# Optimization experiments

Measured on AMD Instinct MI355X. Metric: run time of the kernel, lower is better.

Reference implementation:

```python
import jax, jax.numpy as jnp
import numpy as np
import math

B, S, D, H = 1, 2048, 4096, 32
HD = D // H  # 128
BASE = 10000.0
NEG = -1e9


def rotate_half(x):
    x1, x2 = x[..., : x.shape[-1] // 2], x[..., x.shape[-1] // 2 :]
    return jnp.concatenate((-x2, x1), axis=-1)


def setup_inputs() -> dict:
    key = jax.random.key(0)
    ks = jax.random.split(key, 5)
    scale = 1.0 / math.sqrt(D)
    hidden_states = jax.random.normal(ks[0], (B, S, D), dtype=jnp.float32)
    Wq = jax.random.normal(ks[1], (D, D), dtype=jnp.float32) * scale
    Wk = jax.random.normal(ks[2], (D, D), dtype=jnp.float32) * scale
    Wv = jax.random.normal(ks[3], (D, D), dtype=jnp.float32) * scale
    Wo = jax.random.normal(ks[4], (D, D), dtype=jnp.float32) * scale
    # causal additive mask [1,1,S,S]
    causal = jnp.tril(jnp.ones((S, S), dtype=bool))
    attention_mask = jnp.where(causal, 0.0, NEG).astype(jnp.float32)[None, None]
    # rotary cos/sin cache [1,1,S,HD]
    inv_freq = 1.0 / (BASE ** (jnp.arange(0, HD, 2, dtype=jnp.float32) / HD))
    freqs = jnp.arange(S, dtype=jnp.float32)[:, None] * inv_freq[None, :]
    emb = jnp.concatenate((freqs, freqs), axis=-1)
    cos = jnp.cos(emb)[None, None]
    sin = jnp.sin(emb)[None, None]
    return dict(hidden_states=hidden_states, attention_mask=attention_mask,
                cos=cos, sin=sin, Wq=Wq, Wk=Wk, Wv=Wv, Wo=Wo)


def reference(hidden_states, attention_mask, cos, sin, Wq, Wk, Wv, Wo):
    b, s, d = hidden_states.shape
    # projections (torch Linear: x @ W.T), reshape to [B,H,S,HD]
    def proj(W):
        return (hidden_states @ W.T).reshape(b, s, H, HD).transpose(0, 2, 1, 3)
    q, k, v = proj(Wq), proj(Wk), proj(Wv)
    # RoPE
    q = q * cos + rotate_half(q) * sin
    k = k * cos + rotate_half(k) * sin
    # scores [B,H,S,S], key pre-scaled as in original
    scores = jnp.einsum('bhqd,bhkd->bhqk', q, k / math.sqrt(HD)) + attention_mask
    attn = jax.nn.softmax(scores.astype(jnp.float32), axis=-1).astype(scores.dtype)
    out = jnp.einsum('bhqk,bhkd->bhqd', attn, v)
    out = out.transpose(0, 2, 1, 3).reshape(b, s, d)
    return out @ Wo.T
```

## Files before the change

kernel.cpp:

```cpp
#include <hip/hip_runtime.h>
#include <hip/hip_bf16.h>
#include <stdint.h>

#define DEV __device__ __forceinline__

typedef __bf16 bf16x8 __attribute__((ext_vector_type(8)));
typedef float f32x4 __attribute__((ext_vector_type(4)));
typedef unsigned short ushort8_t __attribute__((ext_vector_type(8)));
typedef unsigned short ushort4_t __attribute__((ext_vector_type(4)));

constexpr int S = 2048;
constexpr int D = 4096;
constexpr int H = 32;
constexpr int HD = 128;
constexpr float kSc = 0.08838834764831845f * 1.4426950408889634f;

DEV unsigned short f2bf(float f) {
    uint32_t u = __builtin_bit_cast(uint32_t, f);
    u += 0x7fffu + ((u >> 16) & 1u);
    return (unsigned short)(u >> 16);
}
DEV float bf2f(unsigned short h) {
    uint32_t u = ((uint32_t)h) << 16;
    return __builtin_bit_cast(float, u);
}

DEV void gload_lds16(const void* g, void* l) {
    __builtin_amdgcn_global_load_lds(
        (const __attribute__((address_space(1))) void*)g,
        (__attribute__((address_space(3))) void*)l,
        16, 0, 0);
}

DEV f32x4 mfma16(bf16x8 a, bf16x8 b, f32x4 c) {
    return __builtin_amdgcn_mfma_f32_16x16x32_bf16(a, b, c, 0, 0, 0);
}

__global__ __launch_bounds__(256) void cvt_all(const float* __restrict__ hs,
                                               const float* __restrict__ w0,
                                               const float* __restrict__ w1,
                                               const float* __restrict__ w2,
                                               const float* __restrict__ w3,
                                               unsigned short* __restrict__ hsb,
                                               unsigned short* __restrict__ o0,
                                               unsigned short* __restrict__ o1,
                                               unsigned short* __restrict__ o2,
                                               unsigned short* __restrict__ o3) {
    const int b = blockIdx.x;
    const float* in;
    unsigned short* out;
    size_t blk;
    if (b < 4096) {
        in = hs; out = hsb; blk = (size_t)b;
    } else {
        const int i = b - 4096;
        const int w = i >> 13;
        const int r = i & 8191;
        in  = (w == 0) ? w0 : (w == 1) ? w1 : (w == 2) ? w2 : w3;
        out = (w == 0) ? o0 : (w == 1) ? o1 : (w == 2) ? o2 : o3;
        blk = (size_t)r;
    }
    const size_t i8 = blk * 256 + threadIdx.x;
    f32x4 a = ((const f32x4*)in)[2 * i8];
    f32x4 c = ((const f32x4*)in)[2 * i8 + 1];
    ushort8_t o;
    o[0] = f2bf(a[0]); o[1] = f2bf(a[1]); o[2] = f2bf(a[2]); o[3] = f2bf(a[3]);
    o[4] = f2bf(c[0]); o[5] = f2bf(c[1]); o[6] = f2bf(c[2]); o[7] = f2bf(c[3]);
    ((ushort8_t*)out)[i8] = o;
}

template <int BN, int OMODE>
__global__ __launch_bounds__(512, 2) void gemm8(const unsigned short* __restrict__ Ap,
                                                const unsigned short* __restrict__ Bp,
                                                unsigned short* __restrict__ Oq,
                                                unsigned short* __restrict__ Ok,
                                                unsigned short* __restrict__ Ovt,
                                                float* __restrict__ Of) {
    constexpr int NT = BN / 64;
    constexpr int NB = BN / 64;
    extern __shared__ unsigned short lds8[];
    unsigned short (*As)[8192] = (unsigned short(*)[8192])lds8;
    unsigned short* Bs0 = lds8 + 4 * 8192;
    unsigned short* Bs1 = Bs0 + BN * 64;

    const int tix = threadIdx.x;
    const int lane = tix & 63;
    const int w = tix >> 6;
    const int g = lane >> 4;
    const int rl = lane & 15;
    const int wm = w >> 2;
    const int wn = w & 3;
    const int bc0 = wn * (BN / 4);
    const int rx = rl & 7;

    const int yy = blockIdx.x & 7;
    const int xx = blockIdx.x >> 3;
    const int m0 = yy * 256;
    const int n0 = xx * BN;

    int srowA[2], scolA[2];
#pragma unroll
    for (int u = 0; u < 2; ++u) {
        const int c = u * 512 + tix;
        srowA[u] = c >> 3;
        scolA[u] = ((c & 7) ^ (srowA[u] & 7)) << 3;
    }
    int srowB[NB], scolB[NB];
#pragma unroll
    for (int u = 0; u < NB; ++u) {
        const int c = u * 512 + tix;
        srowB[u] = c >> 3;
        scolB[u] = ((c & 7) ^ (srowB[u] & 7)) << 3;
    }

    const char* aBase[2] = {(const char*)As[wm], (const char*)As[2 + wm]};
    const char* bBase[2] = {(const char*)Bs0, (const char*)Bs1};

    f32x4 acc[4][2][NT] = {};
    bf16x8 bfr[NT][2];

#define STG_A8(t, h, slot)                                                        \
    if ((t) < 64) {                                                               \
        _Pragma("unroll") for (int u = 0; u < 2; ++u)                             \
            gload_lds16(Ap + (size_t)(m0 + (h) * 128 + srowA[u]) * 4096 +         \
                            (t) * 64 + scolA[u],                                  \
                        &As[slot][(u * 512 + tix) * 8]);                          \
    }
#define STG_B8(t, slot)                                                           \
    if ((t) < 64) {                                                               \
        unsigned short* bs_ = (slot) ? Bs1 : Bs0;                                 \
        _Pragma("unroll") for (int u = 0; u < NB; ++u)                            \
            gload_lds16(Bp + (size_t)(n0 + srowB[u]) * 4096 +                     \
                            (t) * 64 + scolB[u],                                  \
                        &bs_[(u * 512 + tix) * 8]);                               \
    }

#define PHASE8(pt, q, STG, VM)                                                    \
    {                                                                             \
        bf16x8 af[2][2];                                                          \
        _Pragma("unroll") for (int mi = 0; mi < 2; ++mi)                          \
        _Pragma("unroll") for (int ks = 0; ks < 2; ++ks) {                        \
            const int ab = ((q) * 32 + mi * 16 + rl) * 128 +                      \
                           ((((ks << 2) + g) ^ rx) << 4);                         \
            af[mi][ks] = *(const bf16x8*)(aBase[pt] + ab);                        \
        }                                                                         \
        if ((q) == 0) {                                                           \
            _Pragma("unroll") for (int nt = 0; nt < NT; ++nt)                     \
            _Pragma("unroll") for (int ks = 0; ks < 2; ++ks) {                    \
                const int bb = (bc0 + nt * 16 + rl) * 128 +                       \
                               ((((ks << 2) + g) ^ rx) << 4);                     \
                bfr[nt][ks] = *(const bf16x8*)(bBase[pt] + bb);                   \
            }                                                                     \
        }                                                                         \
        STG;                                                                      \
        if (VM) {                                                                 \
            if (last) {                                                           \
                asm volatile("s_waitcnt vmcnt(0)" ::: "memory");                  \
            } else if constexpr (NB == 3) {                                       \
                asm volatile("s_waitcnt vmcnt(3)" ::: "memory");                  \
            } else {                                                              \
                asm volatile("s_waitcnt vmcnt(2)" ::: "memory");                  \
            }                                                                     \
        }                                                                         \
        __builtin_amdgcn_s_barrier();                                             \
        __builtin_amdgcn_s_setprio(1);                                            \
        _Pragma("unroll") for (int ks = 0; ks < 2; ++ks)                          \
        _Pragma("unroll") for (int mi = 0; mi < 2; ++mi)                          \
        _Pragma("unroll") for (int nt = 0; nt < NT; ++nt)                         \
            acc[q][mi][nt] = mfma16(af[mi][ks], bfr[nt][ks], acc[q][mi][nt]);     \
        __builtin_amdgcn_s_setprio(0);                                            \
        __builtin_amdgcn_s_barrier();                                             \
    }

    STG_A8(0, 0, 0); STG_A8(0, 1, 1);
    STG_B8(0, 0); STG_B8(1, 1);
    __syncthreads();

    for (int i = 0; i < 32; ++i) {
        const bool last = (i == 31);
        const int o = 2 * i + 1, ne = 2 * i + 2, no = 2 * i + 3;
        PHASE8(0, 0, STG_A8(o, 0, 2), 0)
        PHASE8(0, 1, STG_A8(o, 1, 3), 0)
        PHASE8(0, 2, STG_B8(ne, 0), 0)
        PHASE8(0, 3, ((void)0), 1)
        PHASE8(1, 0, STG_A8(ne, 0, 0), 0)
        PHASE8(1, 1, STG_A8(ne, 1, 1), 0)
        PHASE8(1, 2, STG_B8(no, 1), 0)
        PHASE8(1, 3, ((void)0), 1)
    }
#undef PHASE8
#undef STG_A8
#undef STG_B8

#pragma unroll
    for (int q = 0; q < 4; ++q)
#pragma unroll
        for (int mi = 0; mi < 2; ++mi)
#pragma unroll
            for (int nt = 0; nt < NT; ++nt) {
                const int row0 = m0 + wm * 128 + q * 32 + mi * 16 + g * 4;
                const int gc = n0 + bc0 + nt * 16 + rl;
                if constexpr (OMODE == 0) {
                    const int sel = gc >> 12;
                    const int col = gc & 4095;
                    if (sel == 2) {
                        ushort4_t v;
#pragma unroll
                        for (int r = 0; r < 4; ++r) v[r] = f2bf(acc[q][mi][nt][r]);
                        *(ushort4_t*)&Ovt[(size_t)col * S + row0] = v;
                    } else {
                        unsigned short* op = sel ? Ok : Oq;
#pragma unroll
                        for (int r = 0; r < 4; ++r)
                            op[(size_t)(row0 + r) * 4096 + col] = f2bf(acc[q][mi][nt][r]);
                    }
                } else {
#pragma unroll
                    for (int r = 0; r < 4; ++r)
                        Of[(size_t)(row0 + r) * 4096 + gc] = acc[q][mi][nt][r];
                }
            }
}

__global__ __launch_bounds__(256) void rope_kernel(unsigned short* __restrict__ Qb,
                                                   unsigned short* __restrict__ Kb,
                                                   const float* __restrict__ cosT,
                                                   const float* __restrict__ sinT) {
    const int i = blockIdx.x * 256 + threadIdx.x;
    const int j8 = i & 7;
    const int h = (i >> 3) & 31;
    const int s = i >> 8;
    const size_t base = (size_t)s * D + h * HD + j8 * 8;
    const float* cp = cosT + s * HD + j8 * 8;
    const float* sp = sinT + s * HD + j8 * 8;
    float c1[8], s1[8], c2[8], s2[8];
#pragma unroll
    for (int k = 0; k < 8; ++k) { c1[k] = cp[k]; s1[k] = sp[k]; c2[k] = cp[k + 64]; s2[k] = sp[k + 64]; }

#pragma unroll
    for (int w = 0; w < 2; ++w) {
        unsigned short* p = (w == 0 ? Qb : Kb) + base;
        const float f = (w == 0) ? kSc : 1.0f;
        ushort8_t x1 = *(ushort8_t*)p;
        ushort8_t x2 = *(ushort8_t*)(p + 64);
        ushort8_t o1, o2;
#pragma unroll
        for (int k = 0; k < 8; ++k) {
            const float a = bf2f(x1[k]);
            const float b = bf2f(x2[k]);
            o1[k] = f2bf((a * c1[k] - b * s1[k]) * f);
            o2[k] = f2bf((b * c2[k] + a * s2[k]) * f);
        }
        *(ushort8_t*)p = o1;
        *(ushort8_t*)(p + 64) = o2;
    }
}

__global__ __launch_bounds__(512, 2) void flash_attn(const unsigned short* __restrict__ Q,
                                                     const unsigned short* __restrict__ K,
                                                     const unsigned short* __restrict__ V,
                                                     unsigned short* __restrict__ O) {
    extern __shared__ unsigned short ldsA[];
    unsigned short* KsB = ldsA;
    unsigned short* VsB = ldsA + 16384;
    unsigned short* PsB = ldsA + 24576;

    const int t = threadIdx.x;
    const int lane = t & 63;
    const int wid = t >> 6;
    const int g = lane >> 4;
    const int rl = lane & 15;
    const int bid = blockIdx.x;
    const int p = 7 - (bid >> 5);
    const int h = bid & 31;
    const int qt = (wid < 4) ? (8 + p) : (7 - p);
    const int wrow0 = qt * 128 + (wid & 3) * 32;

    bf16x8 qf[2][4];
#pragma unroll
    for (int mi = 0; mi < 2; ++mi) {
        const unsigned short* qp = Q + (size_t)(wrow0 + mi * 16 + rl) * D + h * HD;
#pragma unroll
        for (int ks = 0; ks < 4; ++ks) qf[mi][ks] = *(const bf16x8*)(qp + ks * 32 + g * 8);
    }

    f32x4 accO[2][8] = {};
    float m2s[2] = {-1e30f, -1e30f};
    float lsum[2] = {0.f, 0.f};

#pragma unroll
    for (int r = 0; r < 2; ++r) {
        const int c = r * 512 + t;
        const int rowk = c >> 4;
        const int srck = (c & 15) ^ (rowk & 7);
        gload_lds16(K + (size_t)rowk * D + h * HD + srck * 8, &KsB[c * 8]);
    }
    __syncthreads();

    int cur = 0;
    const int ntiles = 2 * (8 + p) + 2;
    for (int kv = 0; kv < ntiles; ++kv) {
        const int kv0 = kv * 64;
#pragma unroll
        for (int r = 0; r < 2; ++r) {
            const int c = r * 512 + t;
            const int rowv = c >> 3;
            const int srcv = (c & 7) ^ (rowv & 7);
            gload_lds16(V + (size_t)(h * HD + rowv) * S + kv0 + srcv * 8, &VsB[c * 8]);
        }
        if (kv + 1 < ntiles) {
#pragma unroll
            for (int r = 0; r < 2; ++r) {
                const int c = r * 512 + t;
                const int rowk = c >> 4;
                const int srck = (c & 15) ^ (rowk & 7);
                gload_lds16(K + (size_t)(kv0 + 64 + rowk) * D + h * HD + srck * 8,
                            &KsB[(cur ^ 1) * 8192 + c * 8]);
            }
        }

        const bool active = kv0 <= wrow0 + 31;
        if (active) {
            const unsigned short* KsC = KsB + cur * 8192;
            f32x4 sf[2][4];
#pragma unroll
            for (int mi = 0; mi < 2; ++mi)
#pragma unroll
                for (int nt = 0; nt < 4; ++nt) sf[mi][nt] = f32x4{0.f, 0.f, 0.f, 0.f};
            __builtin_amdgcn_s_setprio(1);
#pragma unroll
            for (int nt = 0; nt < 4; ++nt) {
                const int row = nt * 16 + rl;
#pragma unroll
                for (int ks = 0; ks < 4; ++ks) {
                    bf16x8 kf = *(const bf16x8*)&KsC[row * 128 + (((ks * 4 + g) ^ (row & 7)) << 3)];
                    sf[0][nt] = mfma16(kf, qf[0][ks], sf[0][nt]);
                    sf[1][nt] = mfma16(kf, qf[1][ks], sf[1][nt]);
                }
            }
            __builtin_amdgcn_s_setprio(0);

            const bool needMask = (kv0 + 63 > wrow0);
            float cf2[2];
            bool chg = false;
#pragma unroll
            for (int mi = 0; mi < 2; ++mi) {
                const int qrow = wrow0 + mi * 16 + rl;
                float mx = -1e30f;
                if (needMask) {
#pragma unroll
                    for (int nt = 0; nt < 4; ++nt)
#pragma unroll
                        for (int r = 0; r < 4; ++r) {
                            const int kcol = kv0 + nt * 16 + g * 4 + r;
                            float s = sf[mi][nt][r];
                            s = (kcol > qrow) ? -1e30f : s;
                            sf[mi][nt][r] = s;
                            mx = fmaxf(mx, s);
                        }
                } else {
#pragma unroll
                    for (int nt = 0; nt < 4; ++nt)
#pragma unroll
                        for (int r = 0; r < 4; ++r) mx = fmaxf(mx, sf[mi][nt][r]);
                }
                mx = fmaxf(mx, __shfl_xor(mx, 16));
                mx = fmaxf(mx, __shfl_xor(mx, 32));
                const float mn = (mx <= m2s[mi] + 8.f) ? m2s[mi] : mx;
                cf2[mi] = __builtin_amdgcn_exp2f(m2s[mi] - mn);
                chg |= (mn > m2s[mi]);
                m2s[mi] = mn;
                float rs = 0.f;
#pragma unroll
                for (int nt = 0; nt < 4; ++nt)
#pragma unroll
                    for (int r = 0; r < 4; ++r) {
                        const float pv = __builtin_amdgcn_exp2f(sf[mi][nt][r] - mn);
                        sf[mi][nt][r] = pv;
                        rs += pv;
                    }
                rs += __shfl_xor(rs, 16);
                rs += __shfl_xor(rs, 32);
                lsum[mi] = lsum[mi] * cf2[mi] + rs;
            }

            if (__any((int)chg)) {
#pragma unroll
                for (int mi = 0; mi < 2; ++mi)
#pragma unroll
                    for (int nt = 0; nt < 8; ++nt)
#pragma unroll
                        for (int r = 0; r < 4; ++r) accO[mi][nt][r] *= cf2[mi];
            }

            unsigned short* myP = PsB + wid * 2048;
#pragma unroll
            for (int mi = 0; mi < 2; ++mi) {
                const int row = mi * 16 + rl;
                const int rxp = row & 7;
#pragma unroll
                for (int nt = 0; nt < 4; ++nt) {
                    ushort4_t v;
#pragma unroll
                    for (int r = 0; r < 4; ++r) v[r] = f2bf(sf[mi][nt][r]);
                    const int chunk = nt * 2 + (g >> 1);
                    *(ushort4_t*)&myP[row * 64 + ((chunk ^ rxp) << 3) + ((g & 1) << 2)] = v;
                }
            }
        }
        __syncthreads();

        if (active) {
            unsigned short* myP = PsB + wid * 2048;
            __builtin_amdgcn_s_setprio(1);
#pragma unroll
            for (int ks = 0; ks < 2; ++ks) {
                bf16x8 pa[2];
#pragma unroll
                for (int mi = 0; mi < 2; ++mi) {
                    const int row = mi * 16 + rl;
                    pa[mi] = *(const bf16x8*)&myP[row * 64 + (((ks * 4 + g) ^ (row & 7)) << 3)];
                }
#pragma unroll
                for (int nt = 0; nt < 8; ++nt) {
                    const int vrow = nt * 16 + rl;
                    bf16x8 vf = *(const bf16x8*)&VsB[vrow * 64 + (((ks * 4 + g) ^ (vrow & 7)) << 3)];
                    accO[0][nt] = mfma16(vf, pa[0], accO[0][nt]);
                    accO[1][nt] = mfma16(vf, pa[1], accO[1][nt]);
                }
            }
            __builtin_amdgcn_s_setprio(0);
        }
        __syncthreads();
        cur ^= 1;
    }

#pragma unroll
    for (int mi = 0; mi < 2; ++mi) {
        const float inv = 1.0f / lsum[mi];
        const int qrow = wrow0 + mi * 16 + rl;
#pragma unroll
        for (int nt = 0; nt < 8; ++nt) {
            ushort4_t v;
#pragma unroll
            for (int r = 0; r < 4; ++r) v[r] = f2bf(accO[mi][nt][r] * inv);
            *(ushort4_t*)&O[(size_t)qrow * D + h * HD + nt * 16 + g * 4] = v;
        }
    }
}

extern "C" void kernel_launch(void* const* d_in, const int* in_sizes, int n_in,
                              void* d_out, int out_size, void* d_ws, size_t ws_size,
                              hipStream_t stream) {
    const float* hs   = (const float*)d_in[0];
    const float* cosT = (const float*)d_in[2];
    const float* sinT = (const float*)d_in[3];
    const float* Wq   = (const float*)d_in[4];
    const float* Wk   = (const float*)d_in[5];
    const float* Wv   = (const float*)d_in[6];
    const float* Wo   = (const float*)d_in[7];

    char* ws = (char*)d_ws;
    const size_t MB = 1ull << 20;
    unsigned short* hsb = (unsigned short*)(ws);
    unsigned short* wqb = (unsigned short*)(ws + 16 * MB);
    unsigned short* wkb = (unsigned short*)(ws + 48 * MB);
    unsigned short* wvb = (unsigned short*)(ws + 80 * MB);
    unsigned short* wob = (unsigned short*)(ws + 112 * MB);
    unsigned short* Qb  = (unsigned short*)(ws + 144 * MB);
    unsigned short* Kb  = (unsigned short*)(ws + 160 * MB);
    unsigned short* Vt  = (unsigned short*)(ws + 176 * MB);
    unsigned short* AOb = (unsigned short*)(ws + 192 * MB);

    cvt_all<<<4096 + 4 * 8192, 256, 0, stream>>>(hs, Wq, Wk, Wv, Wo,
                                                 hsb, wqb, wkb, wvb, wob);

    gemm8<192, 0><<<512, 512, 114688, stream>>>(hsb, wqb, Qb, Kb, Vt, nullptr);

    rope_kernel<<<2048, 256, 0, stream>>>(Qb, Kb, cosT, sinT);

    flash_attn<<<256, 512, 81920, stream>>>(Qb, Kb, Vt, AOb);

    gemm8<128, 1><<<256, 512, 98304, stream>>>(AOb, wob, nullptr, nullptr, nullptr,
                                               (float*)d_out);
}
```

Measured before the change: 414.3 us.

## Add dedicated QKV GEMM kernel with smaller M tile and higher occupancy

Replaces the templated QKV projection GEMM (256x192 tiles, 512 blocks) with a dedicated kernel that uses 128x192 tiles, 1024 blocks, 80KB LDS and a launch bound of 4 blocks per CU. Loads use a double-buffered A/B schedule with a new block-to-tile mapping. The aim is more waves in flight and better load balance across CUs. The trade-off is less operand reuse per tile and more global traffic. The output GEMM and flash attention are only cleaned up, with the same math.

```diff
diff --git a/kernel.cpp b/kernel.cpp
--- a/kernel.cpp
+++ b/kernel.cpp
@@ -69,15 +69,159 @@
     ((ushort8_t*)out)[i8] = o;
 }
 
-template <int BN, int OMODE>
-__global__ __launch_bounds__(512, 2) void gemm8(const unsigned short* __restrict__ Ap,
-                                                const unsigned short* __restrict__ Bp,
-                                                unsigned short* __restrict__ Oq,
-                                                unsigned short* __restrict__ Ok,
-                                                unsigned short* __restrict__ Ovt,
-                                                float* __restrict__ Of) {
-    constexpr int NT = BN / 64;
-    constexpr int NB = BN / 64;
+__global__ __launch_bounds__(512, 4) void gemm_qkv4(const unsigned short* __restrict__ Ap,
+                                                    const unsigned short* __restrict__ Bp,
+                                                    unsigned short* __restrict__ Oq,
+                                                    unsigned short* __restrict__ Ok,
+                                                    unsigned short* __restrict__ Ovt) {
+    extern __shared__ unsigned short ldsX[];
+
+    const int tix = threadIdx.x;
+    const int lane = tix & 63;
+    const int w = tix >> 6;
+    const int g = lane >> 4;
+    const int rl = lane & 15;
+    const int wm = w >> 2;
+    const int wn = w & 3;
+    const int bc0 = wn * 48;
+    const int rx = rl & 7;
+
+    const int bid = blockIdx.x;
+    const int mt = (bid & 7) | ((bid >> 9) << 3);
+    const int nn = (bid >> 3) & 63;
+    const int m0 = mt * 128;
+    const int n0 = nn * 192;
+
+    int srowA[2], scolA[2];
+#pragma unroll
+    for (int u = 0; u < 2; ++u) {
+        const int c = u * 512 + tix;
+        srowA[u] = c >> 3;
+        scolA[u] = ((c & 7) ^ (srowA[u] & 7)) << 3;
+    }
+    int srowB[3], scolB[3];
+#pragma unroll
+    for (int u = 0; u < 3; ++u) {
+        const int c = u * 512 + tix;
+        srowB[u] = c >> 3;
+        scolB[u] = ((c & 7) ^ (srowB[u] & 7)) << 3;
+    }
+
+    f32x4 acc[2][2][3] = {};
+    bf16x8 bfr[3][2];
+
+#define STG_A4(t)                                                                 \
+    {                                                                             \
+        unsigned short* as_ = ldsX + (((t) & 1) << 13);                           \
+        _Pragma("unroll") for (int u = 0; u < 2; ++u)                             \
+            gload_lds16(Ap + (size_t)(m0 + srowA[u]) * 4096 + (t) * 64 + scolA[u],\
+                        &as_[(u * 512 + tix) * 8]);                               \
+    }
+#define STG_B4(t)                                                                 \
+    {                                                                             \
+        unsigned short* bs_ = ldsX + 16384 + (((t) & 1) ? 12288 : 0);             \
+        _Pragma("unroll") for (int u = 0; u < 3; ++u)                             \
+            gload_lds16(Bp + (size_t)(n0 + srowB[u]) * 4096 + (t) * 64 + scolB[u],\
+                        &bs_[(u * 512 + tix) * 8]);                               \
+    }
+
+    STG_A4(0); STG_A4(1); STG_B4(0); STG_B4(1);
+    __syncthreads();
+
+    for (int t = 0; t < 64; ++t) {
+        const char* aB = (const char*)(ldsX + ((t & 1) << 13));
+        const char* bB = (const char*)(ldsX + 16384 + ((t & 1) ? 12288 : 0));
+        {
+            bf16x8 af[2][2];
+#pragma unroll
+            for (int mi = 0; mi < 2; ++mi)
+#pragma unroll
+                for (int ks = 0; ks < 2; ++ks) {
+                    const int ab = (wm * 64 + mi * 16 + rl) * 128 +
+                                   ((((ks << 2) + g) ^ rx) << 4);
+                    af[mi][ks] = *(const bf16x8*)(aB + ab);
+                }
+#pragma unroll
+            for (int nt = 0; nt < 3; ++nt)
+#pragma unroll
+                for (int ks = 0; ks < 2; ++ks) {
+                    const int bb = (bc0 + nt * 16 + rl) * 128 +
+                                   ((((ks << 2) + g) ^ rx) << 4);
+                    bfr[nt][ks] = *(const bf16x8*)(bB + bb);
+                }
+            if (t + 1 < 64) STG_A4(t + 1);
+            __builtin_amdgcn_s_barrier();
+            __builtin_amdgcn_s_setprio(1);
+#pragma unroll
+            for (int ks = 0; ks < 2; ++ks)
+#pragma unroll
+                for (int mi = 0; mi < 2; ++mi)
+#pragma unroll
+                    for (int nt = 0; nt < 3; ++nt)
+                        acc[0][mi][nt] = mfma16(af[mi][ks], bfr[nt][ks], acc[0][mi][nt]);
+            __builtin_amdgcn_s_setprio(0);
+            __builtin_amdgcn_s_barrier();
+        }
+        {
+            bf16x8 af[2][2];
+#pragma unroll
+            for (int mi = 0; mi < 2; ++mi)
+#pragma unroll
+                for (int ks = 0; ks < 2; ++ks) {
+                    const int ab = (wm * 64 + 32 + mi * 16 + rl) * 128 +
+                                   ((((ks << 2) + g) ^ rx) << 4);
+                    af[mi][ks] = *(const bf16x8*)(aB + ab);
+                }
+            if (t + 2 < 64) STG_B4(t + 2);
+            if (t >= 62) {
+                asm volatile("s_waitcnt vmcnt(0)" ::: "memory");
+            } else {
+                asm volatile("s_waitcnt vmcnt(3)" ::: "memory");
+            }
+            __builtin_amdgcn_s_barrier();
+            __builtin_amdgcn_s_setprio(1);
+#pragma unroll
+            for (int ks = 0; ks < 2; ++ks)
+#pragma unroll
+                for (int mi = 0; mi < 2; ++mi)
+#pragma unroll
+                    for (int nt = 0; nt < 3; ++nt)
+                        acc[1][mi][nt] = mfma16(af[mi][ks], bfr[nt][ks], acc[1][mi][nt]);
+            __builtin_amdgcn_s_setprio(0);
+            __builtin_amdgcn_s_barrier();
+        }
+    }
+#undef STG_A4
+#undef STG_B4
+
+#pragma unroll
+    for (int q = 0; q < 2; ++q)
+#pragma unroll
+        for (int mi = 0; mi < 2; ++mi)
+#pragma unroll
+            for (int nt = 0; nt < 3; ++nt) {
+                const int row0 = m0 + wm * 64 + q * 32 + mi * 16 + g * 4;
+                const int gc = n0 + bc0 + nt * 16 + rl;
+                const int sel = gc >> 12;
+                const int col = gc & 4095;
+                if (sel == 2) {
+                    ushort4_t v;
+#pragma unroll
+                    for (int r = 0; r < 4; ++r) v[r] = f2bf(acc[q][mi][nt][r]);
+                    *(ushort4_t*)&Ovt[(size_t)col * S + row0] = v;
+                } else {
+                    unsigned short* op = sel ? Ok : Oq;
+#pragma unroll
+                    for (int r = 0; r < 4; ++r)
+                        op[(size_t)(row0 + r) * 4096 + col] = f2bf(acc[q][mi][nt][r]);
+                }
+            }
+}
+
+__global__ __launch_bounds__(512, 2) void gemm_out8(const unsigned short* __restrict__ Ap,
+                                                    const unsigned short* __restrict__ Bp,
+                                                    float* __restrict__ Of) {
+    constexpr int BN = 128, NT = 2, NB = 2;
     extern __shared__ unsigned short lds8[];
     unsigned short (*As)[8192] = (unsigned short(*)[8192])lds8;
     unsigned short* Bs0 = lds8 + 4 * 8192;
@@ -156,8 +300,6 @@
         if (VM) {                                                                 \
             if (last) {                                                           \
                 asm volatile("s_waitcnt vmcnt(0)" ::: "memory");                  \
-            } else if constexpr (NB == 3) {                                       \
-                asm volatile("s_waitcnt vmcnt(3)" ::: "memory");                  \
             } else {                                                              \
                 asm volatile("s_waitcnt vmcnt(2)" ::: "memory");                  \
             }                                                                     \
@@ -200,25 +342,9 @@
             for (int nt = 0; nt < NT; ++nt) {
                 const int row0 = m0 + wm * 128 + q * 32 + mi * 16 + g * 4;
                 const int gc = n0 + bc0 + nt * 16 + rl;
-                if constexpr (OMODE == 0) {
-                    const int sel = gc >> 12;
-                    const int col = gc & 4095;
-                    if (sel == 2) {
-                        ushort4_t v;
-#pragma unroll
-                        for (int r = 0; r < 4; ++r) v[r] = f2bf(acc[q][mi][nt][r]);
-                        *(ushort4_t*)&Ovt[(size_t)col * S + row0] = v;
-                    } else {
-                        unsigned short* op = sel ? Ok : Oq;
-#pragma unroll
-                        for (int r = 0; r < 4; ++r)
-                            op[(size_t)(row0 + r) * 4096 + col] = f2bf(acc[q][mi][nt][r]);
-                    }
-                } else {
-#pragma unroll
-                    for (int r = 0; r < 4; ++r)
-                        Of[(size_t)(row0 + r) * 4096 + gc] = acc[q][mi][nt][r];
-                }
+#pragma unroll
+                for (int r = 0; r < 4; ++r)
+                    Of[(size_t)(row0 + r) * 4096 + gc] = acc[q][mi][nt][r];
             }
 }
 
@@ -261,9 +387,6 @@
                                                      const unsigned short* __restrict__ V,
                                                      unsigned short* __restrict__ O) {
     extern __shared__ unsigned short ldsA[];
-    unsigned short* KsB = ldsA;
-    unsigned short* VsB = ldsA + 16384;
-    unsigned short* PsB = ldsA + 24576;
 
     const int t = threadIdx.x;
     const int lane = t & 63;
@@ -293,7 +416,7 @@
         const int c = r * 512 + t;
         const int rowk = c >> 4;
         const int srck = (c & 15) ^ (rowk & 7);
-        gload_lds16(K + (size_t)rowk * D + h * HD + srck * 8, &KsB[c * 8]);
+        gload_lds16(K + (size_t)rowk * D + h * HD + srck * 8, &ldsA[c * 8]);
     }
     __syncthreads();
 
@@ -306,7 +429,8 @@
             const int c = r * 512 + t;
             const int rowv = c >> 3;
             const int srcv = (c & 7) ^ (rowv & 7);
-            gload_lds16(V + (size_t)(h * HD + rowv) * S + kv0 + srcv * 8, &VsB[c * 8]);
+            gload_lds16(V + (size_t)(h * HD + rowv) * S + kv0 + srcv * 8,
+                        &ldsA[16384 + c * 8]);
         }
         if (kv + 1 < ntiles) {
 #pragma unroll
@@ -315,13 +439,13 @@
                 const int rowk = c >> 4;
                 const int srck = (c & 15) ^ (rowk & 7);
                 gload_lds16(K + (size_t)(kv0 + 64 + rowk) * D + h * HD + srck * 8,
-                            &KsB[(cur ^ 1) * 8192 + c * 8]);
+                            &ldsA[(cur ^ 1) * 8192 + c * 8]);
             }
         }
 
         const bool active = kv0 <= wrow0 + 31;
         if (active) {
-            const unsigned short* KsC = KsB + cur * 8192;
+            const unsigned short* KsC = ldsA + cur * 8192;
             f32x4 sf[2][4];
 #pragma unroll
             for (int mi = 0; mi < 2; ++mi)
@@ -393,7 +517,7 @@
                         for (int r = 0; r < 4; ++r) accO[mi][nt][r] *= cf2[mi];
             }
 
-            unsigned short* myP = PsB + wid * 2048;
+            unsigned short* myP = ldsA + 24576 + wid * 2048;
 #pragma unroll
             for (int mi = 0; mi < 2; ++mi) {
                 const int row = mi * 16 + rl;
@@ -411,7 +535,8 @@
         __syncthreads();
 
         if (active) {
-            unsigned short* myP = PsB + wid * 2048;
+            unsigned short* myP = ldsA + 24576 + wid * 2048;
+            const unsigned short* VsC = ldsA + 16384;
             __builtin_amdgcn_s_setprio(1);
 #pragma unroll
             for (int ks = 0; ks < 2; ++ks) {
@@ -424,7 +549,7 @@
 #pragma unroll
                 for (int nt = 0; nt < 8; ++nt) {
                     const int vrow = nt * 16 + rl;
-                    bf16x8 vf = *(const bf16x8*)&VsB[vrow * 64 + (((ks * 4 + g) ^ (vrow & 7)) << 3)];
+                    bf16x8 vf = *(const bf16x8*)&VsC[vrow * 64 + (((ks * 4 + g) ^ (vrow & 7)) << 3)];
                     accO[0][nt] = mfma16(vf, pa[0], accO[0][nt]);
                     accO[1][nt] = mfma16(vf, pa[1], accO[1][nt]);
                 }
@@ -475,12 +600,11 @@
     cvt_all<<<4096 + 4 * 8192, 256, 0, stream>>>(hs, Wq, Wk, Wv, Wo,
                                                  hsb, wqb, wkb, wvb, wob);
 
-    gemm8<192, 0><<<512, 512, 114688, stream>>>(hsb, wqb, Qb, Kb, Vt, nullptr);
+    gemm_qkv4<<<1024, 512, 81920, stream>>>(hsb, wqb, Qb, Kb, Vt);
 
     rope_kernel<<<2048, 256, 0, stream>>>(Qb, Kb, cosT, sinT);
 
     flash_attn<<<256, 512, 81920, stream>>>(Qb, Kb, Vt, AOb);
 
-    gemm8<128, 1><<<256, 512, 98304, stream>>>(AOb, wob, nullptr, nullptr, nullptr,
-                                               (float*)d_out);
-}
+    gemm_out8<<<256, 512, 98304, stream>>>(AOb, wob, (float*)d_out);
+}
```

Measured after the change: 458.9 us. +10.8%, slower.
